# Kernel tuning notes

Measured on AMD Instinct MI355X. Metric: run time of the kernel, lower is better.

## Reference

```python
import jax, jax.numpy as jnp
import numpy as np
from jax import lax

SFREQ = 250.0
ORDER = 4
BANDS = [(4.0, 8.0), (8.0, 12.0), (12.0, 16.0), (16.0, 20.0), (20.0, 24.0), (24.0, 28.0), (28.0, 32.0), (32.0, 36.0), (36.0, 40.0)]
KLEN = int(SFREQ // 2)
if KLEN % 2 == 0:
    KLEN += 1  # 125 taps, odd -> same-length output with pad K//2


def _butter_bandpass(order, low, high, sfreq):
    # numpy reimplementation of scipy.signal.butter(order, [low,high]/nyq, btype='band')
    nyq = sfreq / 2.0
    fs = 2.0
    warped = 2.0 * fs * np.tan(np.pi * np.array([low, high]) / nyq / fs)
    m = np.arange(-order + 1, order, 2)
    p = -np.exp(1j * np.pi * m / (2 * order))  # analog Butterworth LP prototype poles
    k = 1.0
    bw = warped[1] - warped[0]
    wo = np.sqrt(warped[0] * warped[1])
    p_lp = p * bw / 2.0
    p_bp = np.concatenate([p_lp + np.sqrt(p_lp ** 2 - wo ** 2), p_lp - np.sqrt(p_lp ** 2 - wo ** 2)])
    z_bp = np.zeros(order, dtype=complex)
    k_bp = k * bw ** order
    fs2 = 2.0 * fs  # bilinear transform
    z_d = (fs2 + z_bp) / (fs2 - z_bp)
    p_d = (fs2 + p_bp) / (fs2 - p_bp)
    z_d = np.append(z_d, -np.ones(len(p_bp) - len(z_bp)))
    k_d = k_bp * np.real(np.prod(fs2 - z_bp) / np.prod(fs2 - p_bp))
    b = np.real(k_d * np.poly(z_d))
    a = np.real(np.poly(p_d))
    return b, a


def _make_kernel(low, high):
    # IIR impulse response (centered impulse, as in the torch module), Hann window, L1 normalize
    b, a = _butter_bandpass(ORDER, low, high, SFREQ)
    x = np.zeros(KLEN)
    x[KLEN // 2] = 1.0
    h = np.zeros(KLEN)
    for n in range(KLEN):
        s = 0.0
        for i in range(len(b)):
            if n - i >= 0:
                s += b[i] * x[n - i]
        for j in range(1, len(a)):
            if n - j >= 0:
                s -= a[j] * h[n - j]
        h[n] = s / a[0]
    nn = np.arange(KLEN)
    h = h * (0.5 - 0.5 * np.cos(2.0 * np.pi * nn / (KLEN - 1)))  # symmetric Hann
    return h / np.sum(np.abs(h))


def setup_inputs() -> dict:
    key = jax.random.key(0)
    x = jax.random.normal(key, (64, 64, 1000), dtype=jnp.float32)  # (B, C, T) EEG
    kernels = jnp.asarray(np.stack([_make_kernel(lo, hi) for lo, hi in BANDS]), dtype=jnp.float32)  # (n_bands, K)
    return {"x": x, "kernels": kernels}


def reference(x, kernels):
    # out[b, i, c, t] = cross-correlation of channel c with band-i kernel (torch Conv1d semantics)
    B, C, T = x.shape
    nb, K = kernels.shape
    pad = K // 2
    x2 = x.reshape(B * C, 1, T)
    w = kernels[:, None, :]  # (n_bands, 1, K)
    y = lax.conv_general_dilated(x2, w, (1,), [(pad, pad)], dimension_numbers=("NCH", "OIH", "NCH"))
    return y.reshape(B, C, nb, T).transpose(0, 2, 1, 3)  # (B, n_bands, C, T)
```

## Files before the change

### kernel.cpp

```cpp
#include <hip/hip_runtime.h>
#include <hip/hip_bf16.h>


#define T_LEN    1000
#define NB       9
#define S_COPY   1160
#define SLOTS    145

typedef __attribute__((ext_vector_type(8))) short short8;
typedef __attribute__((ext_vector_type(4))) float f32x4;

__device__ __forceinline__ unsigned int f2bf(float f) {
    union { __hip_bfloat16 h; unsigned short u; } cv;
    cv.h = __float2bfloat16(f);
    return (unsigned int)cv.u;
}

__global__ __launch_bounds__(256) void fbank_mfma(
    const float* __restrict__ x,
    const float* __restrict__ kern,
    float* __restrict__ out)
{
    __shared__ unsigned short xs[8 * S_COPY];

    const int tid = threadIdx.x;
    const int bc  = blockIdx.x;
    const int b   = bc >> 6, c = bc & 63;
    const float* xrow = x + (size_t)bc * T_LEN;

    {
        const int r = tid >> 5, q0 = tid & 31;
        #pragma unroll
        for (int i = 0; i < 5; ++i) {
            int q = q0 + 32 * i;
            if (q < SLOTS) {
                int idx0 = 8 * q + r - 64;
                unsigned int d[4];
                #pragma unroll
                for (int e2 = 0; e2 < 4; ++e2) {
                    int i0 = idx0 + 2 * e2, i1 = i0 + 1;
                    float v0 = ((unsigned)i0 < T_LEN) ? xrow[i0] : 0.f;
                    float v1 = ((unsigned)i1 < T_LEN) ? xrow[i1] : 0.f;
                    d[e2] = f2bf(v0) | (f2bf(v1) << 16);
                }
                *reinterpret_cast<uint4*>(&xs[r * S_COPY + 8 * q]) =
                    make_uint4(d[0], d[1], d[2], d[3]);
            }
        }
    }

    const int lane = tid & 63;
    const int wid  = tid >> 6;
    const int n = lane & 15, g = lane >> 4;

    short8 bt[4];
    #pragma unroll
    for (int kk = 0; kk < 4; ++kk) {
        unsigned int u[4];
        #pragma unroll
        for (int e2 = 0; e2 < 4; ++e2) {
            int k0 = kk * 32 + 8 * g + 2 * e2;
            float v0 = (n < NB && k0 < 125)     ? kern[n * 125 + k0]     : 0.f;
            float v1 = (n < NB && k0 + 1 < 125) ? kern[n * 125 + k0 + 1] : 0.f;
            u[e2] = f2bf(v0) | (f2bf(v1) << 16);
        }
        union { uint4 u4; short8 s8; } cv;
        cv.u4 = make_uint4(u[0], u[1], u[2], u[3]);
        bt[kk] = cv.s8;
    }

    __syncthreads();

    const int t0w = wid << 8;
    const int rl  = (n + 2) & 7;
    const char* xsb = reinterpret_cast<const char*>(xs);
    const int LB = 2 * (1159 * rl + 2 + n + 8 * g + t0w);

    short8 F[8];
    #pragma unroll
    for (int u = 0; u < 6; ++u)
        F[u] = *reinterpret_cast<const short8*>(xsb + LB + 32 * u);

    const bool bandok = (n < NB);
    float* obase = out + ((size_t)(b * NB + n) * 64 + c) * T_LEN + t0w + 4 * g;

    #pragma unroll
    for (int m = 0; m < 16; ++m) {
        F[(m + 6) & 7] = *reinterpret_cast<const short8*>(xsb + LB + 32 * (m + 6));
        f32x4 acc = {0.f, 0.f, 0.f, 0.f};
        #pragma unroll
        for (int kk = 0; kk < 4; ++kk)
            acc = __builtin_amdgcn_mfma_f32_16x16x32_bf16(F[(m + 2 * kk) & 7], bt[kk], acc, 0, 0, 0);
        const int t4 = t0w + 16 * m + 4 * g;
        if (bandok && t4 + 4 <= T_LEN)
            *reinterpret_cast<f32x4*>(obase + 16 * m) = acc;
    }
}

extern "C" void kernel_launch(void* const* d_in, const int* in_sizes, int n_in,
                              void* d_out, int out_size, void* d_ws, size_t ws_size,
                              hipStream_t stream) {
    const float* x    = (const float*)d_in[0];
    const float* kern = (const float*)d_in[1];
    float* out = (float*)d_out;

    fbank_mfma<<<64 * 64, 256, 0, stream>>>(x, kern, out);
}
```

Before: 60.29 us.

## Stage MFMA outputs through LDS for contiguous 256-byte global stores

```diff
diff --git a/kernel.cpp b/kernel.cpp
--- a/kernel.cpp
+++ b/kernel.cpp
@@ -6,6 +6,7 @@
 #define NB       9
 #define S_COPY   1160
 #define SLOTS    145
+#define STG_W    68
 
 typedef __attribute__((ext_vector_type(8))) short short8;
 typedef __attribute__((ext_vector_type(4))) float f32x4;
@@ -22,6 +23,7 @@
     float* __restrict__ out)
 {
     __shared__ unsigned short xs[8 * S_COPY];
+    __shared__ float stg[4 * NB * STG_W];
 
     const int tid = threadIdx.x;
     const int bc  = blockIdx.x;
@@ -76,24 +78,44 @@
     const char* xsb = reinterpret_cast<const char*>(xs);
     const int LB = 2 * (1159 * rl + 2 + n + 8 * g + t0w);
 
+    float* sw = stg + wid * (NB * STG_W);
+    const bool bandok = (n < NB);
+
     short8 F[8];
     #pragma unroll
     for (int u = 0; u < 6; ++u)
         F[u] = *reinterpret_cast<const short8*>(xsb + LB + 32 * u);
 
-    const bool bandok = (n < NB);
-    float* obase = out + ((size_t)(b * NB + n) * 64 + c) * T_LEN + t0w + 4 * g;
-
     #pragma unroll
-    for (int m = 0; m < 16; ++m) {
-        F[(m + 6) & 7] = *reinterpret_cast<const short8*>(xsb + LB + 32 * (m + 6));
-        f32x4 acc = {0.f, 0.f, 0.f, 0.f};
+    for (int ch = 0; ch < 4; ++ch) {
         #pragma unroll
-        for (int kk = 0; kk < 4; ++kk)
-            acc = __builtin_amdgcn_mfma_f32_16x16x32_bf16(F[(m + 2 * kk) & 7], bt[kk], acc, 0, 0, 0);
-        const int t4 = t0w + 16 * m + 4 * g;
-        if (bandok && t4 + 4 <= T_LEN)
-            *reinterpret_cast<f32x4*>(obase + 16 * m) = acc;
+        for (int pp = 0; pp < 2; ++pp) {
+            const int P = ch * 2 + pp;
+            F[(2 * P + 6) & 7] = *reinterpret_cast<const short8*>(xsb + LB + 32 * (2 * P + 6));
+            F[(2 * P + 7) & 7] = *reinterpret_cast<const short8*>(xsb + LB + 32 * (2 * P + 7));
+            f32x4 ae = {0.f, 0.f, 0.f, 0.f}, ao = {0.f, 0.f, 0.f, 0.f};
+            #pragma unroll
+            for (int kk = 0; kk < 4; ++kk) {
+                ae = __builtin_amdgcn_mfma_f32_16x16x32_bf16(F[(2 * P + 2 * kk) & 7],     bt[kk], ae, 0, 0, 0);
+                ao = __builtin_amdgcn_mfma_f32_16x16x32_bf16(F[(2 * P + 1 + 2 * kk) & 7], bt[kk], ao, 0, 0, 0);
+            }
+            if (bandok) {
+                const int base = n * STG_W + 32 * pp + 4 * g;
+                *reinterpret_cast<f32x4*>(sw + base)      = ae;
+                *reinterpret_cast<f32x4*>(sw + base + 16) = ao;
+            }
+        }
+        const int tcb = t0w + 64 * ch;
+        #pragma unroll
+        for (int it = 0; it < 3; ++it) {
+            int flat = it * 64 + lane;
+            int bb = flat >> 4, cc = flat & 15;
+            if (bb < NB && tcb + 4 * cc + 4 <= T_LEN) {
+                f32x4 v = *reinterpret_cast<const f32x4*>(sw + bb * STG_W + 4 * cc);
+                *reinterpret_cast<f32x4*>(
+                    out + ((size_t)(b * NB + bb) * 64 + c) * T_LEN + tcb + 4 * cc) = v;
+            }
+        }
     }
 }
 
```

Measured after the change: 62.53 us. 3.7% more time.

## Stage filter taps in LDS, remap block order, batch output stores after MFMA loop

Applied to the files above, without the earlier changes.

```diff
diff --git a/kernel.cpp b/kernel.cpp
--- a/kernel.cpp
+++ b/kernel.cpp
@@ -6,6 +6,7 @@
 #define NB       9
 #define S_COPY   1160
 #define SLOTS    145
+#define WT_STRIDE 136
 
 typedef __attribute__((ext_vector_type(8))) short short8;
 typedef __attribute__((ext_vector_type(4))) float f32x4;
@@ -22,11 +23,27 @@
     float* __restrict__ out)
 {
     __shared__ unsigned short xs[8 * S_COPY];
+    __shared__ unsigned short wt[16 * WT_STRIDE];
 
     const int tid = threadIdx.x;
-    const int bc  = blockIdx.x;
+    const int bid = blockIdx.x;
+    const int bc  = ((bid & 7) << 9) + (bid >> 3);
     const int b   = bc >> 6, c = bc & 63;
     const float* xrow = x + (size_t)bc * T_LEN;
+
+    {
+        const int band = tid >> 4, k0 = (tid & 15) << 3;
+        unsigned int d[4];
+        #pragma unroll
+        for (int e2 = 0; e2 < 4; ++e2) {
+            int k = k0 + 2 * e2;
+            float v0 = (band < NB && k < 125)     ? kern[band * 125 + k]     : 0.f;
+            float v1 = (band < NB && k + 1 < 125) ? kern[band * 125 + k + 1] : 0.f;
+            d[e2] = f2bf(v0) | (f2bf(v1) << 16);
+        }
+        *reinterpret_cast<uint4*>(&wt[band * WT_STRIDE + k0]) =
+            make_uint4(d[0], d[1], d[2], d[3]);
+    }
 
     {
         const int r = tid >> 5, q0 = tid & 31;
@@ -53,23 +70,12 @@
     const int wid  = tid >> 6;
     const int n = lane & 15, g = lane >> 4;
 
+    __syncthreads();
+
     short8 bt[4];
     #pragma unroll
-    for (int kk = 0; kk < 4; ++kk) {
-        unsigned int u[4];
-        #pragma unroll
-        for (int e2 = 0; e2 < 4; ++e2) {
-            int k0 = kk * 32 + 8 * g + 2 * e2;
-            float v0 = (n < NB && k0 < 125)     ? kern[n * 125 + k0]     : 0.f;
-            float v1 = (n < NB && k0 + 1 < 125) ? kern[n * 125 + k0 + 1] : 0.f;
-            u[e2] = f2bf(v0) | (f2bf(v1) << 16);
-        }
-        union { uint4 u4; short8 s8; } cv;
-        cv.u4 = make_uint4(u[0], u[1], u[2], u[3]);
-        bt[kk] = cv.s8;
-    }
-
-    __syncthreads();
+    for (int kk = 0; kk < 4; ++kk)
+        bt[kk] = *reinterpret_cast<const short8*>(wt + n * WT_STRIDE + kk * 32 + g * 8);
 
     const int t0w = wid << 8;
     const int rl  = (n + 2) & 7;
@@ -81,19 +87,24 @@
     for (int u = 0; u < 6; ++u)
         F[u] = *reinterpret_cast<const short8*>(xsb + LB + 32 * u);
 
-    const bool bandok = (n < NB);
-    float* obase = out + ((size_t)(b * NB + n) * 64 + c) * T_LEN + t0w + 4 * g;
-
+    f32x4 acc[16];
     #pragma unroll
     for (int m = 0; m < 16; ++m) {
         F[(m + 6) & 7] = *reinterpret_cast<const short8*>(xsb + LB + 32 * (m + 6));
-        f32x4 acc = {0.f, 0.f, 0.f, 0.f};
+        f32x4 a = {0.f, 0.f, 0.f, 0.f};
         #pragma unroll
         for (int kk = 0; kk < 4; ++kk)
-            acc = __builtin_amdgcn_mfma_f32_16x16x32_bf16(F[(m + 2 * kk) & 7], bt[kk], acc, 0, 0, 0);
+            a = __builtin_amdgcn_mfma_f32_16x16x32_bf16(F[(m + 2 * kk) & 7], bt[kk], a, 0, 0, 0);
+        acc[m] = a;
+    }
+
+    const bool bandok = (n < NB);
+    float* obase = out + ((size_t)(b * NB + n) * 64 + c) * T_LEN + t0w + 4 * g;
+    #pragma unroll
+    for (int m = 0; m < 16; ++m) {
         const int t4 = t0w + 16 * m + 4 * g;
         if (bandok && t4 + 4 <= T_LEN)
-            *reinterpret_cast<f32x4*>(obase + 16 * m) = acc;
+            *reinterpret_cast<f32x4*>(obase + 16 * m) = acc[m];
     }
 }
 
```

Result: faster. 56.86 us (-5.7%).
